# Performance work log

Hardware: AMD Instinct MI355X
Metric: run time of the kernel (lower is better)

The kernel has to match this reference:

```python
import jax, jax.numpy as jnp
import numpy as np

DIM = 128
N_NODES = 100000
N_EDGES = 200000
M = 800000  # incidence pairs in each direction
L = 2
N_CLASS = 10


def setup_inputs() -> dict:
    key = jax.random.key(0)
    ks = jax.random.split(key, 8)
    s = 1.0 / np.sqrt(DIM)
    return {
        "node_x": jax.random.normal(ks[0], (N_NODES, DIM), jnp.float32),
        "nodes_map": jax.random.randint(ks[1], (M,), 0, N_NODES, jnp.int32),
        "edge_seg": jnp.sort(jax.random.randint(ks[2], (M,), 0, N_EDGES, jnp.int32)),
        "edges_map": jax.random.randint(ks[3], (M,), 0, N_EDGES, jnp.int32),
        "node_seg": jnp.sort(jax.random.randint(ks[4], (M,), 0, N_NODES, jnp.int32)),
        "num_edges": N_EDGES,
        "W_e": jax.random.normal(ks[5], (L, DIM, DIM), jnp.float32) * s,
        "b_e": jnp.zeros((L, DIM), jnp.float32),
        "g_e": jnp.ones((L, DIM), jnp.float32),
        "be_e": jnp.zeros((L, DIM), jnp.float32),
        "W_n": jax.random.normal(ks[6], (L, DIM, DIM), jnp.float32) * s,
        "b_n": jnp.zeros((L, DIM), jnp.float32),
        "g_n": jnp.ones((L, DIM), jnp.float32),
        "be_n": jnp.zeros((L, DIM), jnp.float32),
        "W_c": jax.random.normal(ks[7], (DIM, N_CLASS), jnp.float32) * s,
        "b_c": jnp.zeros((N_CLASS,), jnp.float32),
    }


def _seg_mean(x, seg, num_segments):
    # global_mean_pool: segment sum / count (count clamped to 1 for empty segments)
    s = jax.ops.segment_sum(x, seg, num_segments=num_segments)
    cnt = jax.ops.segment_sum(jnp.ones((x.shape[0],), x.dtype), seg, num_segments=num_segments)
    return s / jnp.maximum(cnt, 1.0)[:, None]


def _layernorm(x, g, b, eps=1e-5):
    m = jnp.mean(x, axis=-1, keepdims=True)
    v = jnp.mean(jnp.square(x - m), axis=-1, keepdims=True)
    return (x - m) * jax.lax.rsqrt(v + eps) * g + b


def reference(node_x, nodes_map, edge_seg, edges_map, node_seg, num_edges,
              W_e, b_e, g_e, be_e, W_n, b_n, g_n, be_n, W_c, b_c):
    n_nodes = node_x.shape[0]
    x = node_x  # in_drp = Dropout(0.0) is identity
    for i in range(W_e.shape[0]):
        # N2E: gather node feats per (edge, member) pair, mean-pool per hyperedge
        ex = _seg_mean(x[nodes_map], edge_seg, num_edges)          # [E, DIM]
        ex = jax.nn.relu(_layernorm(ex @ W_e[i] + b_e[i], g_e[i], be_e[i]))
        # E2N: gather edge feats per (node, incident-edge) pair, mean-pool per node
        x = _seg_mean(ex[edges_map], node_seg, n_nodes)            # [N, DIM]
        x = jax.nn.relu(_layernorm(x @ W_n[i] + b_n[i], g_n[i], be_n[i]))
    return jax.nn.log_softmax(x @ W_c + b_c, axis=-1)
```

## Files before the change

### kernel.cpp

```cpp
#include <hip/hip_runtime.h>
#include <hip/hip_bf16.h>

#define DIM 128

typedef __bf16 bf16x8 __attribute__((ext_vector_type(8)));
typedef float f32x4 __attribute__((ext_vector_type(4)));

static inline int cdiv(int a, int b) { return (a + b - 1) / b; }
static inline size_t align256(size_t x) { return (x + 255) & ~size_t(255); }

__device__ inline unsigned short f2bf(float f) {
    union { float f; unsigned int u; } v; v.f = f;
    unsigned int r = v.u + 0x7fff + ((v.u >> 16) & 1);
    return (unsigned short)(r >> 16);
}
__device__ inline unsigned int hb(float f) {
    return (__builtin_bit_cast(unsigned int, f) + 0x8000u) >> 16;
}

__global__ void seg_offsets2_kernel(const int* __restrict__ segA, int mA, int nA,
                                    int* __restrict__ offA,
                                    const int* __restrict__ segB, int mB, int nB,
                                    int* __restrict__ offB) {
    int i = blockIdx.x * blockDim.x + threadIdx.x;
    if (i <= nA) {
        int lo = 0, hi = mA;
        while (lo < hi) { int mid = (lo + hi) >> 1; if (segA[mid] < i) lo = mid + 1; else hi = mid; }
        offA[i] = lo;
    }
    int j = i - (nA + 1);
    if (j >= 0 && j <= nB) {
        int lo = 0, hi = mB;
        while (lo < hi) { int mid = (lo + hi) >> 1; if (segB[mid] < j) lo = mid + 1; else hi = mid; }
        offB[j] = lo;
    }
}

__global__ void f32_to_bf16_kernel(const float* __restrict__ in,
                                   unsigned short* __restrict__ out, int n4) {
    int i = blockIdx.x * blockDim.x + threadIdx.x;
    if (i >= n4) return;
    float4 v = ((const float4*)in)[i];
    ushort4 o;
    o.x = f2bf(v.x); o.y = f2bf(v.y); o.z = f2bf(v.z); o.w = f2bf(v.w);
    ((ushort4*)out)[i] = o;
}

__global__ void swizzle_w_kernel(const float* __restrict__ W_e, const float* __restrict__ W_n,
                                 unsigned short* __restrict__ wsw) {
    int gid = blockIdx.x * blockDim.x + threadIdx.x;
    int mi = gid >> 11;
    int e = gid & 2047;
    const float* W = (mi < 2) ? (W_e + (size_t)mi * DIM * DIM)
                              : (W_n + (size_t)(mi - 2) * DIM * DIM);
    int t = e >> 9, n = (e >> 6) & 7, lane = e & 63;
    int q = lane >> 4, c = lane & 15;
    int k0 = t * 32 + q * 8, col = n * 16 + c;
    unsigned short vals[8];
#pragma unroll
    for (int j = 0; j < 8; ++j) vals[j] = f2bf(W[(size_t)(k0 + j) * DIM + col]);
    ushort4* dst = (ushort4*)(wsw + (size_t)gid * 8);
    dst[0] = make_ushort4(vals[0], vals[1], vals[2], vals[3]);
    dst[1] = make_ushort4(vals[4], vals[5], vals[6], vals[7]);
}

__device__ inline void accum8s(float* a, uint4 v, float wt) {
    unsigned int u[4] = {v.x, v.y, v.z, v.w};
#pragma unroll
    for (int i = 0; i < 4; ++i) {
        float lo = __builtin_bit_cast(float, u[i] << 16);
        float hi = __builtin_bit_cast(float, u[i]);
        a[2 * i]     = fmaf(wt, lo, a[2 * i]);
        a[2 * i + 1] = fmaf(wt, hi, a[2 * i + 1]);
    }
}

__global__ __launch_bounds__(512)
void fused_pool_gemm_ln_relu_v7_kernel(const uint4* __restrict__ src,
                                       const int* __restrict__ map,
                                       const int* __restrict__ off,
                                       const unsigned short* __restrict__ Wsw,
                                       const float* __restrict__ b,
                                       const float* __restrict__ g,
                                       const float* __restrict__ be,
                                       unsigned short* __restrict__ Y,
                                       int nseg) {
    __shared__ bf16x8 wlds[2048];
    __shared__ unsigned short alds[128 * 128];
    int tid = threadIdx.x;
    int w = tid >> 6, lane = tid & 63;
    int q = lane >> 4, c = lane & 15;

    {
        const uint4* gsrc = (const uint4*)Wsw;
        uint4* ldst = (uint4*)wlds;
#pragma unroll
        for (int i = 0; i < 4; ++i) ldst[tid + i * 512] = gsrc[tid + i * 512];
    }

    int blockbase = blockIdx.x * 128;
    int wavebase = w * 16;

    float bcol[8], gcol[8], becol[8];
#pragma unroll
    for (int n = 0; n < 8; ++n) {
        int col = n * 16 + c;
        bcol[n] = b[col]; gcol[n] = g[col]; becol[n] = be[col];
    }
    int begv[4], endv[4];
#pragma unroll
    for (int it = 0; it < 4; ++it) {
        int sc = min(blockbase + wavebase + it * 4 + q, nseg - 1);
        begv[it] = off[sc];
        endv[it] = off[sc + 1];
    }

    __syncthreads();

    const char* sbase = (const char*)src;
    unsigned cb = (unsigned)(c << 4);
    for (int it = 0; it < 4; ++it) {
        int s_local = wavebase + it * 4 + q;
        int beg = begv[it], end = endv[it];
        int e1 = max(end - 1, 0);
        float a[8] = {0.f, 0.f, 0.f, 0.f, 0.f, 0.f, 0.f, 0.f};
        unsigned r0 = (unsigned)map[min(beg, e1)];
        unsigned r1 = (unsigned)map[min(beg + 1, e1)];
        unsigned r2 = (unsigned)map[min(beg + 2, e1)];
        unsigned r3 = (unsigned)map[min(beg + 3, e1)];
        for (int j = beg; j < end; j += 4) {
            uint4 v0 = *(const uint4*)(sbase + ((r0 << 8) + cb));
            uint4 v1 = *(const uint4*)(sbase + ((r1 << 8) + cb));
            uint4 v2 = *(const uint4*)(sbase + ((r2 << 8) + cb));
            uint4 v3 = *(const uint4*)(sbase + ((r3 << 8) + cb));
            int jn = j + 4;
            unsigned n0 = (unsigned)map[min(jn, e1)];
            unsigned n1 = (unsigned)map[min(jn + 1, e1)];
            unsigned n2 = (unsigned)map[min(jn + 2, e1)];
            unsigned n3 = (unsigned)map[min(jn + 3, e1)];
            accum8s(a, v0, 1.f);
            accum8s(a, v1, (j + 1 < end) ? 1.f : 0.f);
            accum8s(a, v2, (j + 2 < end) ? 1.f : 0.f);
            accum8s(a, v3, (j + 3 < end) ? 1.f : 0.f);
            r0 = n0; r1 = n1; r2 = n2; r3 = n3;
        }
        float inv = 1.f / fmaxf((float)(end - beg), 1.f);
        uint4 o;
        o.x = hb(a[0] * inv) | (hb(a[1] * inv) << 16);
        o.y = hb(a[2] * inv) | (hb(a[3] * inv) << 16);
        o.z = hb(a[4] * inv) | (hb(a[5] * inv) << 16);
        o.w = hb(a[6] * inv) | (hb(a[7] * inv) << 16);
        uint4* wrow = (uint4*)(alds + (size_t)s_local * 128);
        wrow[c ^ (s_local & 7)] = o;
    }

    f32x4 acc[8];
#pragma unroll
    for (int n = 0; n < 8; ++n) acc[n] = f32x4{bcol[n], bcol[n], bcol[n], bcol[n]};

    const uint4* arow = (const uint4*)(alds + (size_t)(wavebase + c) * 128);
    int key = c & 7;
    bf16x8 a0 = *(const bf16x8*)&arow[(q + 0) ^ key];
    bf16x8 a1 = *(const bf16x8*)&arow[(q + 4) ^ key];
    bf16x8 a2 = *(const bf16x8*)&arow[(q + 8) ^ key];
    bf16x8 a3 = *(const bf16x8*)&arow[(q + 12) ^ key];

#pragma unroll
    for (int n = 0; n < 8; ++n) {
        acc[n] = __builtin_amdgcn_mfma_f32_16x16x32_bf16(a0, wlds[(0 * 8 + n) * 64 + lane], acc[n], 0, 0, 0);
        acc[n] = __builtin_amdgcn_mfma_f32_16x16x32_bf16(a1, wlds[(1 * 8 + n) * 64 + lane], acc[n], 0, 0, 0);
        acc[n] = __builtin_amdgcn_mfma_f32_16x16x32_bf16(a2, wlds[(2 * 8 + n) * 64 + lane], acc[n], 0, 0, 0);
        acc[n] = __builtin_amdgcn_mfma_f32_16x16x32_bf16(a3, wlds[(3 * 8 + n) * 64 + lane], acc[n], 0, 0, 0);
    }

    float s1[4], s2[4];
#pragma unroll
    for (int j = 0; j < 4; ++j) {
        float t1 = 0.f, t2 = 0.f;
#pragma unroll
        for (int n = 0; n < 8; ++n) { float v = acc[n][j]; t1 += v; t2 = fmaf(v, v, t2); }
        s1[j] = t1; s2[j] = t2;
    }
#pragma unroll
    for (int o = 1; o < 16; o <<= 1)
#pragma unroll
        for (int j = 0; j < 4; ++j) {
            s1[j] += __shfl_xor(s1[j], o);
            s2[j] += __shfl_xor(s2[j], o);
        }

#pragma unroll
    for (int j = 0; j < 4; ++j) {
        int row = blockbase + wavebase + q * 4 + j;
        if (row >= nseg) continue;
        float m = s1[j] * (1.f / DIM);
        float var = fmaf(-m, m, s2[j] * (1.f / DIM));
        float inv = rsqrtf(var + 1e-5f);
        unsigned short* yp = Y + (size_t)row * DIM + c;
#pragma unroll
        for (int n = 0; n < 8; ++n) {
            float d = acc[n][j] - m;
            float y = fmaxf(fmaf(d * inv, gcol[n], becol[n]), 0.f);
            unsigned int u = __builtin_bit_cast(unsigned int, y) + 0x8000u;
            yp[n * 16] = (unsigned short)(u >> 16);
        }
    }
}

#define CL_ROWS 4
__global__ __launch_bounds__(256)
void classifier_logsoftmax_v3_kernel(const uint4* __restrict__ X,
                                     const float* __restrict__ Wc,
                                     const float* __restrict__ bc,
                                     float* __restrict__ out, int nrows) {
    int w = threadIdx.x >> 6, lane = threadIdx.x & 63;
    int g = lane >> 4, c16 = lane & 15;
    int r0 = (blockIdx.x * 16 + w * 4 + g) * CL_ROWS;
    if (r0 >= nrows) return;

    float wc[8][10];
#pragma unroll
    for (int j = 0; j < 8; ++j)
#pragma unroll
        for (int c = 0; c < 10; ++c) wc[j][c] = Wc[(c16 * 8 + j) * 10 + c];
    float bcv[10];
#pragma unroll
    for (int c = 0; c < 10; ++c) bcv[c] = bc[c];

    int rend = min(r0 + CL_ROWS, nrows);
    for (int r = r0; r < rend; ++r) {
        uint4 v = X[(size_t)r * 16 + c16];
        float x[8];
        {
            unsigned int u[4] = {v.x, v.y, v.z, v.w};
#pragma unroll
            for (int i = 0; i < 4; ++i) {
                union { unsigned int ui; float f; } lo, hi;
                lo.ui = u[i] << 16;
                hi.ui = u[i] & 0xffff0000u;
                x[2 * i] = lo.f; x[2 * i + 1] = hi.f;
            }
        }
        float acc[10];
#pragma unroll
        for (int c = 0; c < 10; ++c) acc[c] = 0.f;
#pragma unroll
        for (int j = 0; j < 8; ++j)
#pragma unroll
            for (int c = 0; c < 10; ++c) acc[c] = fmaf(x[j], wc[j][c], acc[c]);

#pragma unroll
        for (int o = 1; o < 16; o <<= 1)
#pragma unroll
            for (int c = 0; c < 10; ++c) acc[c] += __shfl_xor(acc[c], o);

#pragma unroll
        for (int c = 0; c < 10; ++c) acc[c] += bcv[c];

        float mx = acc[0];
#pragma unroll
        for (int c = 1; c < 10; ++c) mx = fmaxf(mx, acc[c]);
        float se = 0.f;
#pragma unroll
        for (int c = 0; c < 10; ++c) se += expf(acc[c] - mx);
        float lse = mx + logf(se);

        float myv = 0.f;
#pragma unroll
        for (int c = 0; c < 10; ++c) myv = (c16 == c) ? acc[c] : myv;
        if (c16 < 10) out[(size_t)r * 10 + c16] = myv - lse;
    }
}

extern "C" void kernel_launch(void* const* d_in, const int* in_sizes, int n_in,
                              void* d_out, int out_size, void* d_ws, size_t ws_size,
                              hipStream_t stream) {
    const float* node_x    = (const float*)d_in[0];
    const int*   nodes_map = (const int*)d_in[1];
    const int*   edge_seg  = (const int*)d_in[2];
    const int*   edges_map = (const int*)d_in[3];
    const int*   node_seg  = (const int*)d_in[4];
    const float* W_e = (const float*)d_in[6];
    const float* b_e = (const float*)d_in[7];
    const float* g_e = (const float*)d_in[8];
    const float* be_e= (const float*)d_in[9];
    const float* W_n = (const float*)d_in[10];
    const float* b_n = (const float*)d_in[11];
    const float* g_n = (const float*)d_in[12];
    const float* be_n= (const float*)d_in[13];
    const float* W_c = (const float*)d_in[14];
    const float* b_c = (const float*)d_in[15];
    float* out = (float*)d_out;

    const int N = in_sizes[0] / DIM;
    const int M = in_sizes[1];
    const int E = 200000;
    const int L = in_sizes[6] / (DIM * DIM);

    char* ws = (char*)d_ws;
    int* edge_off = (int*)ws;           ws += align256((size_t)(E + 1) * sizeof(int));
    int* node_off = (int*)ws;           ws += align256((size_t)(N + 1) * sizeof(int));
    unsigned short* wsw = (unsigned short*)ws;      ws += align256((size_t)4 * 2048 * 8 * sizeof(unsigned short));
    unsigned short* node_xb = (unsigned short*)ws;  ws += align256((size_t)N * DIM * sizeof(unsigned short));
    unsigned short* exb = (unsigned short*)ws;      ws += align256((size_t)E * DIM * sizeof(unsigned short));
    unsigned short* xb  = (unsigned short*)ws;      ws += align256((size_t)N * DIM * sizeof(unsigned short));
    (void)ws_size;

    seg_offsets2_kernel<<<cdiv(E + N + 2, 256), 256, 0, stream>>>(
        edge_seg, M, E, edge_off, node_seg, M, N, node_off);
    f32_to_bf16_kernel<<<cdiv(N * DIM / 4, 256), 256, 0, stream>>>(node_x, node_xb, N * DIM / 4);
    swizzle_w_kernel<<<32, 256, 0, stream>>>(W_e, W_n, wsw);

    const unsigned short* xcur = node_xb;
    for (int i = 0; i < L; ++i) {
        fused_pool_gemm_ln_relu_v7_kernel<<<cdiv(E, 128), 512, 0, stream>>>(
            (const uint4*)xcur, nodes_map, edge_off, wsw + (size_t)i * 16384,
            b_e + i * DIM, g_e + i * DIM, be_e + i * DIM, exb, E);
        fused_pool_gemm_ln_relu_v7_kernel<<<cdiv(N, 128), 512, 0, stream>>>(
            (const uint4*)exb, edges_map, node_off, wsw + (size_t)(2 + i) * 16384,
            b_n + i * DIM, g_n + i * DIM, be_n + i * DIM, xb, N);
        xcur = xb;
    }

    classifier_logsoftmax_v3_kernel<<<cdiv(N, 16 * CL_ROWS), 256, 0, stream>>>(
        (const uint4*)xcur, W_c, b_c, out, N);
}
```

Before: 345.3 us.

## Pool directly into MFMA A-fragment registers and merge setup kernels

The pooling stage now maps each lane to one segment row (lane's c) and a k-quarter (q), so the gathered sums land directly in the bf16x8 A operands for the MFMA. This removes the 32 KB LDS staging buffer and its swizzled write/read round trip, and drops the 4-way unrolled gather in favour of a one-row-per-iteration loop with a prefetched index. Each lane now issues four 16-byte loads per row at strides of 64 bytes instead of one, which changes coalescing and memory-level parallelism. The three setup kernels (segment offsets, input bf16 conversion, weight swizzle) are folded into a single launch to save launch overhead.

```diff
diff --git a/kernel.cpp b/kernel.cpp
--- a/kernel.cpp
+++ b/kernel.cpp
@@ -18,65 +18,64 @@
     return (__builtin_bit_cast(unsigned int, f) + 0x8000u) >> 16;
 }
 
-__global__ void seg_offsets2_kernel(const int* __restrict__ segA, int mA, int nA,
-                                    int* __restrict__ offA,
-                                    const int* __restrict__ segB, int mB, int nB,
-                                    int* __restrict__ offB) {
-    int i = blockIdx.x * blockDim.x + threadIdx.x;
-    if (i <= nA) {
-        int lo = 0, hi = mA;
-        while (lo < hi) { int mid = (lo + hi) >> 1; if (segA[mid] < i) lo = mid + 1; else hi = mid; }
-        offA[i] = lo;
-    }
-    int j = i - (nA + 1);
-    if (j >= 0 && j <= nB) {
-        int lo = 0, hi = mB;
-        while (lo < hi) { int mid = (lo + hi) >> 1; if (segB[mid] < j) lo = mid + 1; else hi = mid; }
-        offB[j] = lo;
-    }
-}
-
-__global__ void f32_to_bf16_kernel(const float* __restrict__ in,
-                                   unsigned short* __restrict__ out, int n4) {
-    int i = blockIdx.x * blockDim.x + threadIdx.x;
-    if (i >= n4) return;
-    float4 v = ((const float4*)in)[i];
-    ushort4 o;
-    o.x = f2bf(v.x); o.y = f2bf(v.y); o.z = f2bf(v.z); o.w = f2bf(v.w);
-    ((ushort4*)out)[i] = o;
-}
-
-__global__ void swizzle_w_kernel(const float* __restrict__ W_e, const float* __restrict__ W_n,
+__global__ void setup_all_kernel(const int* __restrict__ segA, int mA, int nA,
+                                 int* __restrict__ offA,
+                                 const int* __restrict__ segB, int mB, int nB,
+                                 int* __restrict__ offB,
+                                 const float* __restrict__ xin,
+                                 unsigned short* __restrict__ xout, int n4,
+                                 const float* __restrict__ W_e,
+                                 const float* __restrict__ W_n,
                                  unsigned short* __restrict__ wsw) {
     int gid = blockIdx.x * blockDim.x + threadIdx.x;
-    int mi = gid >> 11;
-    int e = gid & 2047;
-    const float* W = (mi < 2) ? (W_e + (size_t)mi * DIM * DIM)
-                              : (W_n + (size_t)(mi - 2) * DIM * DIM);
-    int t = e >> 9, n = (e >> 6) & 7, lane = e & 63;
-    int q = lane >> 4, c = lane & 15;
-    int k0 = t * 32 + q * 8, col = n * 16 + c;
-    unsigned short vals[8];
-#pragma unroll
-    for (int j = 0; j < 8; ++j) vals[j] = f2bf(W[(size_t)(k0 + j) * DIM + col]);
-    ushort4* dst = (ushort4*)(wsw + (size_t)gid * 8);
-    dst[0] = make_ushort4(vals[0], vals[1], vals[2], vals[3]);
-    dst[1] = make_ushort4(vals[4], vals[5], vals[6], vals[7]);
-}
-
-__device__ inline void accum8s(float* a, uint4 v, float wt) {
+
+    if (gid < n4) {
+        float4 v = ((const float4*)xin)[gid];
+        ushort4 o;
+        o.x = f2bf(v.x); o.y = f2bf(v.y); o.z = f2bf(v.z); o.w = f2bf(v.w);
+        ((ushort4*)xout)[gid] = o;
+    }
+
+    if (gid <= nA) {
+        int lo = 0, hi = mA;
+        while (lo < hi) { int mid = (lo + hi) >> 1; if (segA[mid] < gid) lo = mid + 1; else hi = mid; }
+        offA[gid] = lo;
+    }
+    int jj = gid - (nA + 1);
+    if (jj >= 0 && jj <= nB) {
+        int lo = 0, hi = mB;
+        while (lo < hi) { int mid = (lo + hi) >> 1; if (segB[mid] < jj) lo = mid + 1; else hi = mid; }
+        offB[jj] = lo;
+    }
+
+    if (gid < 8192) {
+        int mi = gid >> 11;
+        int e = gid & 2047;
+        const float* W = (mi < 2) ? (W_e + (size_t)mi * DIM * DIM)
+                                  : (W_n + (size_t)(mi - 2) * DIM * DIM);
+        int t = e >> 9, n = (e >> 6) & 7, lane = e & 63;
+        int q = lane >> 4, c = lane & 15;
+        int k0 = t * 32 + q * 8, col = n * 16 + c;
+        unsigned short vals[8];
+#pragma unroll
+        for (int j = 0; j < 8; ++j) vals[j] = f2bf(W[(size_t)(k0 + j) * DIM + col]);
+        ushort4* dst = (ushort4*)(wsw + (size_t)gid * 8);
+        dst[0] = make_ushort4(vals[0], vals[1], vals[2], vals[3]);
+        dst[1] = make_ushort4(vals[4], vals[5], vals[6], vals[7]);
+    }
+}
+
+__device__ inline void accum8(float* a, uint4 v) {
     unsigned int u[4] = {v.x, v.y, v.z, v.w};
 #pragma unroll
     for (int i = 0; i < 4; ++i) {
-        float lo = __builtin_bit_cast(float, u[i] << 16);
-        float hi = __builtin_bit_cast(float, u[i]);
-        a[2 * i]     = fmaf(wt, lo, a[2 * i]);
-        a[2 * i + 1] = fmaf(wt, hi, a[2 * i + 1]);
+        a[2 * i]     += __builtin_bit_cast(float, u[i] << 16);
+        a[2 * i + 1] += __builtin_bit_cast(float, u[i]);
     }
 }
 
 __global__ __launch_bounds__(512)
-void fused_pool_gemm_ln_relu_v7_kernel(const uint4* __restrict__ src,
+void fused_pool_gemm_ln_relu_v8_kernel(const uint4* __restrict__ src,
                                        const int* __restrict__ map,
                                        const int* __restrict__ off,
                                        const unsigned short* __restrict__ Wsw,
@@ -86,7 +85,6 @@
                                        unsigned short* __restrict__ Y,
                                        int nseg) {
     __shared__ bf16x8 wlds[2048];
-    __shared__ unsigned short alds[128 * 128];
     int tid = threadIdx.x;
     int w = tid >> 6, lane = tid & 63;
     int q = lane >> 4, c = lane & 15;
@@ -99,78 +97,61 @@
     }
 
     int blockbase = blockIdx.x * 128;
-    int wavebase = w * 16;
-
-    float bcol[8], gcol[8], becol[8];
+    int seg = min(blockbase + w * 16 + c, nseg - 1);
+    int beg = off[seg], end = off[seg + 1];
+    int e1 = max(end - 1, 0);
+    unsigned r = (unsigned)map[min(beg, e1)];
+
+    __syncthreads();
+
+    float a[4][8];
+#pragma unroll
+    for (int t = 0; t < 4; ++t)
+#pragma unroll
+        for (int i = 0; i < 8; ++i) a[t][i] = 0.f;
+
+    const char* sbase = (const char*)src;
+    unsigned qb = (unsigned)(q << 4);
+    for (int j = beg; j < end; ++j) {
+        const char* p = sbase + ((r << 8) + qb);
+        uint4 v0 = *(const uint4*)(p);
+        uint4 v1 = *(const uint4*)(p + 64);
+        uint4 v2 = *(const uint4*)(p + 128);
+        uint4 v3 = *(const uint4*)(p + 192);
+        unsigned rn = (unsigned)map[min(j + 1, e1)];
+        accum8(a[0], v0);
+        accum8(a[1], v1);
+        accum8(a[2], v2);
+        accum8(a[3], v3);
+        r = rn;
+    }
+
+    float inv = 1.f / fmaxf((float)(end - beg), 1.f);
+    bf16x8 af[4];
+#pragma unroll
+    for (int t = 0; t < 4; ++t) {
+        uint4 o;
+        o.x = hb(a[t][0] * inv) | (hb(a[t][1] * inv) << 16);
+        o.y = hb(a[t][2] * inv) | (hb(a[t][3] * inv) << 16);
+        o.z = hb(a[t][4] * inv) | (hb(a[t][5] * inv) << 16);
+        o.w = hb(a[t][6] * inv) | (hb(a[t][7] * inv) << 16);
+        af[t] = __builtin_bit_cast(bf16x8, o);
+    }
+
+    float bcol[8];
+#pragma unroll
+    for (int n = 0; n < 8; ++n) bcol[n] = b[n * 16 + c];
+
+    f32x4 acc[8];
+#pragma unroll
+    for (int n = 0; n < 8; ++n) acc[n] = f32x4{bcol[n], bcol[n], bcol[n], bcol[n]};
+
 #pragma unroll
     for (int n = 0; n < 8; ++n) {
-        int col = n * 16 + c;
-        bcol[n] = b[col]; gcol[n] = g[col]; becol[n] = be[col];
-    }
-    int begv[4], endv[4];
-#pragma unroll
-    for (int it = 0; it < 4; ++it) {
-        int sc = min(blockbase + wavebase + it * 4 + q, nseg - 1);
-        begv[it] = off[sc];
-        endv[it] = off[sc + 1];
-    }
-
-    __syncthreads();
-
-    const char* sbase = (const char*)src;
-    unsigned cb = (unsigned)(c << 4);
-    for (int it = 0; it < 4; ++it) {
-        int s_local = wavebase + it * 4 + q;
-        int beg = begv[it], end = endv[it];
-        int e1 = max(end - 1, 0);
-        float a[8] = {0.f, 0.f, 0.f, 0.f, 0.f, 0.f, 0.f, 0.f};
-        unsigned r0 = (unsigned)map[min(beg, e1)];
-        unsigned r1 = (unsigned)map[min(beg + 1, e1)];
-        unsigned r2 = (unsigned)map[min(beg + 2, e1)];
-        unsigned r3 = (unsigned)map[min(beg + 3, e1)];
-        for (int j = beg; j < end; j += 4) {
-            uint4 v0 = *(const uint4*)(sbase + ((r0 << 8) + cb));
-            uint4 v1 = *(const uint4*)(sbase + ((r1 << 8) + cb));
-            uint4 v2 = *(const uint4*)(sbase + ((r2 << 8) + cb));
-            uint4 v3 = *(const uint4*)(sbase + ((r3 << 8) + cb));
-            int jn = j + 4;
-            unsigned n0 = (unsigned)map[min(jn, e1)];
-            unsigned n1 = (unsigned)map[min(jn + 1, e1)];
-            unsigned n2 = (unsigned)map[min(jn + 2, e1)];
-            unsigned n3 = (unsigned)map[min(jn + 3, e1)];
-            accum8s(a, v0, 1.f);
-            accum8s(a, v1, (j + 1 < end) ? 1.f : 0.f);
-            accum8s(a, v2, (j + 2 < end) ? 1.f : 0.f);
-            accum8s(a, v3, (j + 3 < end) ? 1.f : 0.f);
-            r0 = n0; r1 = n1; r2 = n2; r3 = n3;
-        }
-        float inv = 1.f / fmaxf((float)(end - beg), 1.f);
-        uint4 o;
-        o.x = hb(a[0] * inv) | (hb(a[1] * inv) << 16);
-        o.y = hb(a[2] * inv) | (hb(a[3] * inv) << 16);
-        o.z = hb(a[4] * inv) | (hb(a[5] * inv) << 16);
-        o.w = hb(a[6] * inv) | (hb(a[7] * inv) << 16);
-        uint4* wrow = (uint4*)(alds + (size_t)s_local * 128);
-        wrow[c ^ (s_local & 7)] = o;
-    }
-
-    f32x4 acc[8];
-#pragma unroll
-    for (int n = 0; n < 8; ++n) acc[n] = f32x4{bcol[n], bcol[n], bcol[n], bcol[n]};
-
-    const uint4* arow = (const uint4*)(alds + (size_t)(wavebase + c) * 128);
-    int key = c & 7;
-    bf16x8 a0 = *(const bf16x8*)&arow[(q + 0) ^ key];
-    bf16x8 a1 = *(const bf16x8*)&arow[(q + 4) ^ key];
-    bf16x8 a2 = *(const bf16x8*)&arow[(q + 8) ^ key];
-    bf16x8 a3 = *(const bf16x8*)&arow[(q + 12) ^ key];
-
-#pragma unroll
-    for (int n = 0; n < 8; ++n) {
-        acc[n] = __builtin_amdgcn_mfma_f32_16x16x32_bf16(a0, wlds[(0 * 8 + n) * 64 + lane], acc[n], 0, 0, 0);
-        acc[n] = __builtin_amdgcn_mfma_f32_16x16x32_bf16(a1, wlds[(1 * 8 + n) * 64 + lane], acc[n], 0, 0, 0);
-        acc[n] = __builtin_amdgcn_mfma_f32_16x16x32_bf16(a2, wlds[(2 * 8 + n) * 64 + lane], acc[n], 0, 0, 0);
-        acc[n] = __builtin_amdgcn_mfma_f32_16x16x32_bf16(a3, wlds[(3 * 8 + n) * 64 + lane], acc[n], 0, 0, 0);
+        acc[n] = __builtin_amdgcn_mfma_f32_16x16x32_bf16(af[0], wlds[(0 * 8 + n) * 64 + lane], acc[n], 0, 0, 0);
+        acc[n] = __builtin_amdgcn_mfma_f32_16x16x32_bf16(af[1], wlds[(1 * 8 + n) * 64 + lane], acc[n], 0, 0, 0);
+        acc[n] = __builtin_amdgcn_mfma_f32_16x16x32_bf16(af[2], wlds[(2 * 8 + n) * 64 + lane], acc[n], 0, 0, 0);
+        acc[n] = __builtin_amdgcn_mfma_f32_16x16x32_bf16(af[3], wlds[(3 * 8 + n) * 64 + lane], acc[n], 0, 0, 0);
     }
 
     float s1[4], s2[4];
@@ -189,18 +170,25 @@
             s2[j] += __shfl_xor(s2[j], o);
         }
 
+    float gcol[8], becol[8];
+#pragma unroll
+    for (int n = 0; n < 8; ++n) {
+        int col = n * 16 + c;
+        gcol[n] = g[col]; becol[n] = be[col];
+    }
+
 #pragma unroll
     for (int j = 0; j < 4; ++j) {
-        int row = blockbase + wavebase + q * 4 + j;
+        int row = blockbase + w * 16 + q * 4 + j;
         if (row >= nseg) continue;
         float m = s1[j] * (1.f / DIM);
         float var = fmaf(-m, m, s2[j] * (1.f / DIM));
-        float inv = rsqrtf(var + 1e-5f);
+        float invs = rsqrtf(var + 1e-5f);
         unsigned short* yp = Y + (size_t)row * DIM + c;
 #pragma unroll
         for (int n = 0; n < 8; ++n) {
             float d = acc[n][j] - m;
-            float y = fmaxf(fmaf(d * inv, gcol[n], becol[n]), 0.f);
+            float y = fmaxf(fmaf(d * invs, gcol[n], becol[n]), 0.f);
             unsigned int u = __builtin_bit_cast(unsigned int, y) + 0x8000u;
             yp[n * 16] = (unsigned short)(u >> 16);
         }
@@ -306,17 +294,16 @@
     unsigned short* xb  = (unsigned short*)ws;      ws += align256((size_t)N * DIM * sizeof(unsigned short));
     (void)ws_size;
 
-    seg_offsets2_kernel<<<cdiv(E + N + 2, 256), 256, 0, stream>>>(
-        edge_seg, M, E, edge_off, node_seg, M, N, node_off);
-    f32_to_bf16_kernel<<<cdiv(N * DIM / 4, 256), 256, 0, stream>>>(node_x, node_xb, N * DIM / 4);
-    swizzle_w_kernel<<<32, 256, 0, stream>>>(W_e, W_n, wsw);
+    setup_all_kernel<<<cdiv(N * DIM / 4, 256), 256, 0, stream>>>(
+        edge_seg, M, E, edge_off, node_seg, M, N, node_off,
+        node_x, node_xb, N * DIM / 4, W_e, W_n, wsw);
 
     const unsigned short* xcur = node_xb;
     for (int i = 0; i < L; ++i) {
-        fused_pool_gemm_ln_relu_v7_kernel<<<cdiv(E, 128), 512, 0, stream>>>(
+        fused_pool_gemm_ln_relu_v8_kernel<<<cdiv(E, 128), 512, 0, stream>>>(
             (const uint4*)xcur, nodes_map, edge_off, wsw + (size_t)i * 16384,
             b_e + i * DIM, g_e + i * DIM, be_e + i * DIM, exb, E);
-        fused_pool_gemm_ln_relu_v7_kernel<<<cdiv(N, 128), 512, 0, stream>>>(
+        fused_pool_gemm_ln_relu_v8_kernel<<<cdiv(N, 128), 512, 0, stream>>>(
             (const uint4*)exb, edges_map, node_off, wsw + (size_t)(2 + i) * 16384,
             b_n + i * DIM, g_n + i * DIM, be_n + i * DIM, xb, N);
         xcur = xb;
```

Measured after the change: 337.9 us. -2.1%, faster.
